# Optimization experiments

Measured on AMD Instinct MI355X. Metric: run time of the kernel, lower is better.

Reference implementation:

```python
import jax, jax.numpy as jnp
import numpy as np


def _conv(x, w, b=None, stride=1, pad=0):
    y = jax.lax.conv_general_dilated(x, w, (stride, stride), [(pad, pad), (pad, pad)],
                                     dimension_numbers=('NCHW', 'OIHW', 'NCHW'))
    if b is not None:
        y = y + b[None, :, None, None]
    return y


def _slice3d(grid, guide):
    # Trilinear grid_sample, align_corners=False, zero padding.
    # grid: (N, C=12, D=8, GH, GW); guide: (N,1,H,W) in [-1,1]
    N, C, D, GH, GW = grid.shape
    H, W = guide.shape[2], guide.shape[3]
    xs = 2.0 * jnp.arange(W, dtype=grid.dtype) / max(W - 1, 1) - 1.0
    ys = 2.0 * jnp.arange(H, dtype=grid.dtype) / max(H - 1, 1) - 1.0
    gx = ((xs + 1.0) * GW - 1.0) * 0.5               # (W,)
    gy = ((ys + 1.0) * GH - 1.0) * 0.5               # (H,)
    gz = ((guide[:, 0] + 1.0) * D - 1.0) * 0.5       # (N,H,W)
    x0f = jnp.floor(gx); y0f = jnp.floor(gy); z0f = jnp.floor(gz)
    fx = gx - x0f; fy = gy - y0f; fz = gz - z0f
    x0 = x0f.astype(jnp.int32); y0 = y0f.astype(jnp.int32); z0 = z0f.astype(jnp.int32)
    gf = grid.reshape(N, C, D * GH * GW)

    def corner(zi, yi, xi, wz, wy, wx):
        mask = ((zi >= 0) & (zi < D)) & ((yi >= 0) & (yi < GH))[None, :, None] & ((xi >= 0) & (xi < GW))[None, None, :]
        zc = jnp.clip(zi, 0, D - 1); yc = jnp.clip(yi, 0, GH - 1); xc = jnp.clip(xi, 0, GW - 1)
        flat = zc * (GH * GW) + yc[None, :, None] * GW + xc[None, None, :]   # (N,H,W)
        v = jnp.take_along_axis(gf, flat.reshape(N, 1, H * W), axis=2).reshape(N, C, H, W)
        w = (wz * wy[None, :, None] * wx[None, None, :]) * mask.astype(grid.dtype)  # (N,H,W)
        return v * w[:, None]

    out = jnp.zeros((N, C, H, W), grid.dtype)
    for dz in (0, 1):
        for dy in (0, 1):
            for dx in (0, 1):
                out = out + corner(z0 + dz, y0 + dy, x0 + dx,
                                   fz if dz else 1.0 - fz,
                                   fy if dy else 1.0 - fy,
                                   fx if dx else 1.0 - fx)
    return out


def setup_inputs() -> dict:
    key = jax.random.key(0)
    ks = jax.random.split(key, 40)
    def w(i, shape):
        return jax.random.normal(ks[i], shape, jnp.float32) * 0.05
    return {
        'low_res': jax.random.uniform(ks[0], (4, 3, 256, 256), jnp.float32),
        'full_res': jax.random.uniform(ks[1], (4, 1, 1024, 1024), jnp.float32),
        'w0': w(2, (8, 3, 3, 3)), 'b0': w(3, (8,)),
        'w1': w(4, (16, 8, 3, 3)), 'b1': w(5, (16,)),
        'w2': w(6, (32, 16, 3, 3)), 'b2': w(7, (32,)),
        'w3': w(8, (64, 32, 3, 3)), 'b3': w(9, (64,)),
        'wl0': w(10, (64, 64, 3, 3)), 'bl0': w(11, (64,)),
        'wl1': w(12, (64, 64, 3, 3)),
        'wg1': w(13, (128, 64, 3, 3)), 'bg1': w(14, (128,)),
        'wg2': w(15, (256, 128, 3, 3)), 'bg2': w(16, (256,)),
        'wf1': w(17, (256, 448, 1, 1)), 'bf1': w(18, (256,)),
        'wf2': w(19, (128, 256, 1, 1)), 'bf2': w(20, (128,)),
        'wf3': w(21, (64, 128, 1, 1)), 'bf3': w(22, (64,)),
        'wlin': w(23, (96, 64, 1, 1)), 'blin': w(24, (96,)),
        'wgd1': w(25, (16, 1, 3, 3)), 'bgd1': w(26, (16,)),
        'wgd2': w(27, (1, 16, 1, 1)), 'bgd2': w(28, (1,)),
        'wau1': w(29, (16, 1, 1, 1)), 'bau1': w(30, (16,)),
        'wau2': w(31, (1, 16, 1, 1)), 'bau2': w(32, (1,)),
        'wav1': w(33, (16, 1, 1, 1)), 'bav1': w(34, (16,)),
        'wav2': w(35, (1, 16, 1, 1)), 'bav2': w(36, (1,)),
    }


def reference(low_res, full_res, w0, b0, w1, b1, w2, b2, w3, b3, wl0, bl0, wl1,
              wg1, bg1, wg2, bg2, wf1, bf1, wf2, bf2, wf3, bf3, wlin, blin,
              wgd1, bgd1, wgd2, bgd2, wau1, bau1, wau2, bau2, wav1, bav1, wav2, bav2):
    relu = jax.nn.relu
    N = low_res.shape[0]
    H, W = full_res.shape[2], full_res.shape[3]
    fake = jax.image.resize(low_res, (N, 3, H, W), 'bilinear')
    # splat stack: 4 stride-2 convs
    x = relu(_conv(low_res, w0, b0, 2, 1))
    x = relu(_conv(x, w1, b1, 2, 1))
    x = relu(_conv(x, w2, b2, 2, 1))
    splat = relu(_conv(x, w3, b3, 2, 1))                 # (N,64,16,16)
    local = _conv(relu(_conv(splat, wl0, bl0, 1, 1)), wl1, None, 1, 1)
    # global branch
    a0 = splat.mean(axis=(2, 3), keepdims=True)
    x1 = relu(_conv(splat, wg1, bg1, 2, 1))
    a1 = x1.mean(axis=(2, 3), keepdims=True)
    x2 = relu(_conv(x1, wg2, bg2, 2, 1))
    a2 = x2.mean(axis=(2, 3), keepdims=True)
    a = jnp.concatenate([a0, a1, a2], axis=1)            # (N,448,1,1)
    a = relu(_conv(a, wf1, bf1))
    a = relu(_conv(a, wf2, bf2))
    glob = relu(_conv(a, wf3, bf3))                      # (N,64,1,1)
    fused = relu(glob + local)
    fused = _conv(fused, wlin, blin)                     # (N,96,16,16)
    grid = fused.reshape(N, 12, 8, fused.shape[2], fused.shape[3])
    guidemap = jnp.tanh(_conv(relu(_conv(full_res, wgd1, bgd1, 1, 1)), wgd2, bgd2))
    coeff = _slice3d(grid, guidemap)                     # (N,12,H,W)
    Y = full_res * coeff[:, 3:4] + coeff[:, 0:3].sum(axis=1, keepdims=True)
    U0 = full_res * coeff[:, 7:8] + coeff[:, 4:7].sum(axis=1, keepdims=True)
    V0 = full_res * coeff[:, 11:12] + coeff[:, 8:11].sum(axis=1, keepdims=True)
    U = jnp.tanh(_conv(relu(_conv(U0, wau1, bau1)), wau2, bau2)) + fake[:, 1:2]
    V = jnp.tanh(_conv(relu(_conv(V0, wav1, bav1)), wav2, bav2)) + fake[:, 2:3]
    return jnp.concatenate([Y, U, V], axis=1)
```

## Files before the change

### kernel.cpp

```cpp
#include <hip/hip_runtime.h>
#include <math.h>


__device__ __forceinline__ float tanh_fast(float x) {
    float e = __expf(2.0f * x);
    return 1.0f - 2.0f / (e + 1.0f);
}

__global__ __launch_bounds__(256) void conv3x3_s2_relu(
    const float* __restrict__ in, const float* __restrict__ w,
    const float* __restrict__ b, float* __restrict__ out,
    int N, int Cin, int Hin, int Win, int Cout, int Hout, int Wout)
{
    int idx = blockIdx.x * blockDim.x + threadIdx.x;
    int total = N * Cout * Hout * Wout;
    if (idx >= total) return;
    int wo = idx % Wout; int t = idx / Wout;
    int ho = t % Hout; t /= Hout;
    int co = t % Cout; int n = t / Cout;
    float acc = b[co];
    int hi0 = ho * 2 - 1, wi0 = wo * 2 - 1;
    const float* wp = w + (size_t)co * Cin * 9;
    for (int ci = 0; ci < Cin; ++ci) {
        const float* ip = in + ((size_t)(n * Cin + ci)) * Hin * Win;
        const float* wc = wp + ci * 9;
        #pragma unroll
        for (int kh = 0; kh < 3; ++kh) {
            int hi = hi0 + kh;
            if ((unsigned)hi >= (unsigned)Hin) continue;
            const float* row = ip + hi * Win;
            #pragma unroll
            for (int kw = 0; kw < 3; ++kw) {
                int wi = wi0 + kw;
                if ((unsigned)wi >= (unsigned)Win) continue;
                acc = fmaf(wc[kh * 3 + kw], row[wi], acc);
            }
        }
    }
    out[idx] = fmaxf(acc, 0.0f);
}

template<int CIN, int STRIDE, bool RELU, bool HASB>
__global__ __launch_bounds__(256) void conv_split(
    const float* __restrict__ in, const float* __restrict__ w,
    const float* __restrict__ b, float* __restrict__ out,
    int Cout, int Hin, int Win, int Hout, int Wout)
{
    constexpr int CPT = CIN / 4;
    int part = threadIdx.x >> 6;
    int lane = threadIdx.x & 63;
    int o = (blockIdx.x << 6) | lane;
    int wo = o % Wout; int t = o / Wout;
    int ho = t % Hout; t /= Hout;
    int co = t % Cout; int n = t / Cout;
    int hi0 = ho * STRIDE - 1, wi0 = wo * STRIDE - 1;
    const float* wp = w + ((size_t)co * CIN + part * CPT) * 9;
    const float* ip = in + ((size_t)n * CIN + part * CPT) * Hin * Win;
    float acc = 0.0f;
    for (int ci = 0; ci < CPT; ++ci) {
        const float* ic = ip + (size_t)ci * Hin * Win;
        const float* wc = wp + ci * 9;
        #pragma unroll
        for (int kh = 0; kh < 3; ++kh) {
            int hi = hi0 + kh;
            if ((unsigned)hi >= (unsigned)Hin) continue;
            const float* row = ic + hi * Win;
            #pragma unroll
            for (int kw = 0; kw < 3; ++kw) {
                int wi = wi0 + kw;
                if ((unsigned)wi >= (unsigned)Win) continue;
                acc = fmaf(wc[kh * 3 + kw], row[wi], acc);
            }
        }
    }
    __shared__ float red[256];
    red[threadIdx.x] = acc;
    __syncthreads();
    if (part == 0) {
        float s = acc + red[64 + lane] + red[128 + lane] + red[192 + lane];
        if (HASB) s += b[co];
        if (RELU) s = fmaxf(s, 0.0f);
        out[o] = s;
    }
}

__global__ __launch_bounds__(256) void means_kernel(
    const float* __restrict__ splat, const float* __restrict__ x1,
    const float* __restrict__ x2, float* __restrict__ avec)
{
    int wid = blockIdx.x * 4 + (threadIdx.x >> 6);
    int lane = threadIdx.x & 63;
    int n = wid / 448; int c = wid % 448;
    float s = 0.0f; float scale;
    if (c < 64) {
        const float* p = splat + ((size_t)(n * 64 + c)) * 256;
        s = p[lane] + p[lane + 64] + p[lane + 128] + p[lane + 192];
        scale = 1.0f / 256.0f;
    } else if (c < 192) {
        const float* p = x1 + ((size_t)(n * 128 + (c - 64))) * 64;
        s = p[lane];
        scale = 1.0f / 64.0f;
    } else {
        const float* p = x2 + ((size_t)(n * 256 + (c - 192))) * 16;
        s = (lane < 16) ? p[lane] : 0.0f;
        scale = 1.0f / 16.0f;
    }
    #pragma unroll
    for (int off = 32; off; off >>= 1) s += __shfl_down(s, off, 64);
    if (lane == 0) avec[wid] = s * scale;
}

template<int INDIM>
__global__ __launch_bounds__(256) void fc_relu(
    const float* __restrict__ in, const float* __restrict__ w,
    const float* __restrict__ b, float* __restrict__ out, int rows)
{
    int wid = blockIdx.x * 4 + (threadIdx.x >> 6);
    int lane = threadIdx.x & 63;
    int row = wid % rows; int n = wid / rows;
    const float* wp = w + (size_t)row * INDIM;
    const float* ip = in + (size_t)n * INDIM;
    float s = 0.0f;
    #pragma unroll
    for (int i = lane; i < INDIM; i += 64) s = fmaf(wp[i], ip[i], s);
    #pragma unroll
    for (int off = 32; off; off >>= 1) s += __shfl_down(s, off, 64);
    if (lane == 0) out[n * rows + row] = fmaxf(s + b[row], 0.0f);
}

__global__ __launch_bounds__(256) void fuse_grid(
    const float* __restrict__ glob, const float* __restrict__ local,
    const float* __restrict__ wlin, const float* __restrict__ blin,
    float* __restrict__ grid)
{
    int idx = blockIdx.x * blockDim.x + threadIdx.x;
    int p = idx & 255; int k = (idx >> 8) % 96; int n = idx / (96 * 256);
    float acc = blin[k];
    const float* wp = wlin + k * 64;
    const float* gl = glob + n * 64;
    const float* lo = local + (size_t)n * 64 * 256 + p;
    for (int c = 0; c < 64; ++c)
        acc = fmaf(wp[c], fmaxf(gl[c] + lo[c * 256], 0.0f), acc);
    int ch = k >> 3; int z = k & 7;
    grid[(((size_t)(n * 8 + z)) * 256 + p) * 12 + ch] = acc;
}

__global__ __launch_bounds__(256) void hdr_out_v2(
    const float* __restrict__ full, const float* __restrict__ low,
    const float* __restrict__ grid,
    const float* __restrict__ wgd1, const float* __restrict__ bgd1,
    const float* __restrict__ wgd2, const float* __restrict__ bgd2,
    const float* __restrict__ wau1, const float* __restrict__ bau1,
    const float* __restrict__ wau2, const float* __restrict__ bau2,
    const float* __restrict__ wav1, const float* __restrict__ bav1,
    const float* __restrict__ wav2, const float* __restrict__ bav2,
    float* __restrict__ out)
{
    int tid = blockIdx.x * 256 + threadIdx.x;
    int x0 = (tid & 255) << 2;
    int y = (tid >> 8) & 1023;
    int n = tid >> 18;
    const float* fp = full + ((size_t)n << 20);

    float v[3][6];
    #pragma unroll
    for (int r = 0; r < 3; ++r) {
        int yy = y + r - 1;
        bool okr = (unsigned)yy < 1024u;
        const float* row = fp + (size_t)yy * 1024;
        if (okr) {
            float4 m = *(const float4*)(row + x0);
            v[r][1] = m.x; v[r][2] = m.y; v[r][3] = m.z; v[r][4] = m.w;
            v[r][0] = (x0 > 0) ? row[x0 - 1] : 0.0f;
            v[r][5] = (x0 < 1020) ? row[x0 + 4] : 0.0f;
        } else {
            #pragma unroll
            for (int j = 0; j < 6; ++j) v[r][j] = 0.0f;
        }
    }

    float gacc[4];
    float bb = bgd2[0];
    #pragma unroll
    for (int px = 0; px < 4; ++px) gacc[px] = bb;
    #pragma unroll
    for (int k = 0; k < 16; ++k) {
        const float* wk = wgd1 + k * 9;
        float w0 = wk[0], w1 = wk[1], w2 = wk[2];
        float w3 = wk[3], w4 = wk[4], w5 = wk[5];
        float w6 = wk[6], w7 = wk[7], w8 = wk[8];
        float bk = bgd1[k], wo = wgd2[k];
        #pragma unroll
        for (int px = 0; px < 4; ++px) {
            float h = bk;
            h = fmaf(w0, v[0][px], h); h = fmaf(w1, v[0][px + 1], h); h = fmaf(w2, v[0][px + 2], h);
            h = fmaf(w3, v[1][px], h); h = fmaf(w4, v[1][px + 1], h); h = fmaf(w5, v[1][px + 2], h);
            h = fmaf(w6, v[2][px], h); h = fmaf(w7, v[2][px + 1], h); h = fmaf(w8, v[2][px + 2], h);
            gacc[px] = fmaf(wo, fmaxf(h, 0.0f), gacc[px]);
        }
    }

    const float* gbase = grid + (size_t)n * 24576;
    float Yo[4], Uo[4], Vo[4];

    #pragma unroll
    for (int px = 0; px < 4; ++px) {
        int x = x0 + px;
        float g = tanh_fast(gacc[px]);

        float gxc = (x * (32.0f / 1023.0f) - 1.0f) * 0.5f;
        float gyc = (y * (32.0f / 1023.0f) - 1.0f) * 0.5f;
        float gzc = 4.0f * g + 3.5f;
        float x0f = floorf(gxc), y0f = floorf(gyc), z0f = floorf(gzc);
        float fx = gxc - x0f, fy = gyc - y0f, fz = gzc - z0f;
        int ix = (int)x0f, iy = (int)y0f, iz = (int)z0f;

        float wx0 = (ix >= 0 && ix < 16) ? (1.0f - fx) : 0.0f;
        float wx1 = (ix + 1 >= 0 && ix + 1 < 16) ? fx : 0.0f;
        float wy0 = (iy >= 0 && iy < 16) ? (1.0f - fy) : 0.0f;
        float wy1 = (iy + 1 >= 0 && iy + 1 < 16) ? fy : 0.0f;
        float wz0 = (iz >= 0 && iz < 8) ? (1.0f - fz) : 0.0f;
        float wz1 = (iz + 1 >= 0 && iz + 1 < 8) ? fz : 0.0f;
        int xi0 = min(max(ix, 0), 15), xi1 = min(max(ix + 1, 0), 15);
        int yi0 = min(max(iy, 0), 15), yi1 = min(max(iy + 1, 0), 15);
        int zi0 = min(max(iz, 0), 7),  zi1 = min(max(iz + 1, 0), 7);

        float w00 = wy0 * wx0, w01 = wy0 * wx1, w10 = wy1 * wx0, w11 = wy1 * wx1;
        int o00 = yi0 * 16 + xi0, o01 = yi0 * 16 + xi1;
        int o10 = yi1 * 16 + xi0, o11 = yi1 * 16 + xi1;
        int z0b = zi0 * 256, z1b = zi1 * 256;

        float acc[12];
        #pragma unroll
        for (int i = 0; i < 12; ++i) acc[i] = 0.0f;

        #define CORNER(OFF, WK) { \
            const float4* q = (const float4*)(gbase + (size_t)(OFF) * 12); \
            float wk_ = (WK); \
            float4 A = q[0], B = q[1], C = q[2]; \
            acc[0] = fmaf(wk_, A.x, acc[0]); acc[1] = fmaf(wk_, A.y, acc[1]); \
            acc[2] = fmaf(wk_, A.z, acc[2]); acc[3] = fmaf(wk_, A.w, acc[3]); \
            acc[4] = fmaf(wk_, B.x, acc[4]); acc[5] = fmaf(wk_, B.y, acc[5]); \
            acc[6] = fmaf(wk_, B.z, acc[6]); acc[7] = fmaf(wk_, B.w, acc[7]); \
            acc[8] = fmaf(wk_, C.x, acc[8]); acc[9] = fmaf(wk_, C.y, acc[9]); \
            acc[10] = fmaf(wk_, C.z, acc[10]); acc[11] = fmaf(wk_, C.w, acc[11]); }

        CORNER(z0b + o00, wz0 * w00)
        CORNER(z0b + o01, wz0 * w01)
        CORNER(z0b + o10, wz0 * w10)
        CORNER(z0b + o11, wz0 * w11)
        CORNER(z1b + o00, wz1 * w00)
        CORNER(z1b + o01, wz1 * w01)
        CORNER(z1b + o10, wz1 * w10)
        CORNER(z1b + o11, wz1 * w11)
        #undef CORNER

        float p = v[1][px + 1];
        float Yv = fmaf(p, acc[3],  acc[0] + acc[1] + acc[2]);
        float U0 = fmaf(p, acc[7],  acc[4] + acc[5] + acc[6]);
        float V0 = fmaf(p, acc[11], acc[8] + acc[9] + acc[10]);

        float uacc = bau2[0];
        #pragma unroll
        for (int k = 0; k < 16; ++k)
            uacc = fmaf(wau2[k], fmaxf(fmaf(wau1[k], U0, bau1[k]), 0.0f), uacc);
        float vacc = bav2[0];
        #pragma unroll
        for (int k = 0; k < 16; ++k)
            vacc = fmaf(wav2[k], fmaxf(fmaf(wav1[k], V0, bav1[k]), 0.0f), vacc);

        float sx = (x + 0.5f) * 0.25f - 0.5f;
        float sy = (y + 0.5f) * 0.25f - 0.5f;
        float sxf = floorf(sx), syf = floorf(sy);
        float fxl = sx - sxf, fyl = sy - syf;
        int jx0 = max((int)sxf, 0), jx1 = min((int)sxf + 1, 255);
        int jy0 = max((int)syf, 0), jy1 = min((int)syf + 1, 255);
        const float* lr1 = low + ((size_t)(n * 3 + 1)) * 65536;
        const float* lr2 = low + ((size_t)(n * 3 + 2)) * 65536;
        float f1 = (1.0f - fyl) * ((1.0f - fxl) * lr1[jy0 * 256 + jx0] + fxl * lr1[jy0 * 256 + jx1])
                 + fyl * ((1.0f - fxl) * lr1[jy1 * 256 + jx0] + fxl * lr1[jy1 * 256 + jx1]);
        float f2 = (1.0f - fyl) * ((1.0f - fxl) * lr2[jy0 * 256 + jx0] + fxl * lr2[jy0 * 256 + jx1])
                 + fyl * ((1.0f - fxl) * lr2[jy1 * 256 + jx0] + fxl * lr2[jy1 * 256 + jx1]);

        Yo[px] = Yv;
        Uo[px] = tanh_fast(uacc) + f1;
        Vo[px] = tanh_fast(vacc) + f2;
    }

    size_t base = ((size_t)n * 3) * 1048576 + (size_t)y * 1024 + x0;
    *(float4*)(out + base)            = make_float4(Yo[0], Yo[1], Yo[2], Yo[3]);
    *(float4*)(out + base + 1048576)  = make_float4(Uo[0], Uo[1], Uo[2], Uo[3]);
    *(float4*)(out + base + 2097152)  = make_float4(Vo[0], Vo[1], Vo[2], Vo[3]);
}

extern "C" void kernel_launch(void* const* d_in, const int* in_sizes, int n_in,
                              void* d_out, int out_size, void* d_ws, size_t ws_size,
                              hipStream_t stream)
{
    const float* low  = (const float*)d_in[0];
    const float* full = (const float*)d_in[1];
    const float* w0 = (const float*)d_in[2];  const float* b0 = (const float*)d_in[3];
    const float* w1 = (const float*)d_in[4];  const float* b1 = (const float*)d_in[5];
    const float* w2 = (const float*)d_in[6];  const float* b2 = (const float*)d_in[7];
    const float* w3 = (const float*)d_in[8];  const float* b3 = (const float*)d_in[9];
    const float* wl0 = (const float*)d_in[10]; const float* bl0 = (const float*)d_in[11];
    const float* wl1 = (const float*)d_in[12];
    const float* wg1 = (const float*)d_in[13]; const float* bg1 = (const float*)d_in[14];
    const float* wg2 = (const float*)d_in[15]; const float* bg2 = (const float*)d_in[16];
    const float* wf1 = (const float*)d_in[17]; const float* bf1 = (const float*)d_in[18];
    const float* wf2 = (const float*)d_in[19]; const float* bf2 = (const float*)d_in[20];
    const float* wf3 = (const float*)d_in[21]; const float* bf3 = (const float*)d_in[22];
    const float* wlin = (const float*)d_in[23]; const float* blin = (const float*)d_in[24];
    const float* wgd1 = (const float*)d_in[25]; const float* bgd1 = (const float*)d_in[26];
    const float* wgd2 = (const float*)d_in[27]; const float* bgd2 = (const float*)d_in[28];
    const float* wau1 = (const float*)d_in[29]; const float* bau1 = (const float*)d_in[30];
    const float* wau2 = (const float*)d_in[31]; const float* bau2 = (const float*)d_in[32];
    const float* wav1 = (const float*)d_in[33]; const float* bav1 = (const float*)d_in[34];
    const float* wav2 = (const float*)d_in[35]; const float* bav2 = (const float*)d_in[36];
    float* out = (float*)d_out;

    float* ws = (float*)d_ws;
    float* t0    = ws;
    float* t1    = t0 + 524288;
    float* t2    = t1 + 262144;
    float* splat = t2 + 131072;
    float* l0o   = splat + 65536;
    float* local = l0o + 65536;
    float* x1    = local + 65536;
    float* x2    = x1 + 32768;
    float* avec  = x2 + 16384;
    float* h1    = avec + 1792;
    float* h2    = h1 + 1024;
    float* glob  = h2 + 512;
    float* gridb = glob + 256;

    conv3x3_s2_relu<<<2048, 256, 0, stream>>>(low, w0, b0, t0, 4, 3, 256, 256, 8, 128, 128);
    conv3x3_s2_relu<<<1024, 256, 0, stream>>>(t0, w1, b1, t1, 4, 8, 128, 128, 16, 64, 64);
    conv_split<16, 2, true, true><<<2048, 256, 0, stream>>>(t1, w2, b2, t2, 32, 64, 64, 32, 32);
    conv_split<32, 2, true, true><<<1024, 256, 0, stream>>>(t2, w3, b3, splat, 64, 32, 32, 16, 16);
    conv_split<64, 1, true, true><<<1024, 256, 0, stream>>>(splat, wl0, bl0, l0o, 64, 16, 16, 16, 16);
    conv_split<64, 1, false, false><<<1024, 256, 0, stream>>>(l0o, wl1, nullptr, local, 64, 16, 16, 16, 16);
    conv_split<64, 2, true, true><<<512, 256, 0, stream>>>(splat, wg1, bg1, x1, 128, 16, 16, 8, 8);
    conv_split<128, 2, true, true><<<256, 256, 0, stream>>>(x1, wg2, bg2, x2, 256, 8, 8, 4, 4);
    means_kernel<<<448, 256, 0, stream>>>(splat, x1, x2, avec);
    fc_relu<448><<<256, 256, 0, stream>>>(avec, wf1, bf1, h1, 256);
    fc_relu<256><<<128, 256, 0, stream>>>(h1, wf2, bf2, h2, 128);
    fc_relu<128><<<64, 256, 0, stream>>>(h2, wf3, bf3, glob, 64);
    fuse_grid<<<384, 256, 0, stream>>>(glob, local, wlin, blin, gridb);
    hdr_out_v2<<<4096, 256, 0, stream>>>(full, low, gridb,
        wgd1, bgd1, wgd2, bgd2, wau1, bau1, wau2, bau2, wav1, bav1, wav2, bav2, out);
}
```

Baseline: 393.8 us.

## Fuse whole HDRNet pipeline into one persistent kernel with grid barriers

Replaces fourteen separate kernel launches with a single persistent kernel of 1024 blocks that walks through every stage and separates them with atomic-counter grid barriers. Independent conv branches are merged into the same phase, the three FC layers are collapsed into one per-batch block using shared memory, and the low-res bilinear upsample in the output stage is simplified to reuse three column samples across four pixels. This removes launch gaps and tail effects between small kernels, but relies on all 1024 blocks being co-resident for the spin barriers to work and forces a fixed grid size on the large output stage.

```diff
diff --git a/kernel.cpp b/kernel.cpp
--- a/kernel.cpp
+++ b/kernel.cpp
@@ -1,25 +1,38 @@
 #include <hip/hip_runtime.h>
 #include <math.h>
 
+
+#define NB 1024
+#define GSZ (NB * 256)
 
 __device__ __forceinline__ float tanh_fast(float x) {
     float e = __expf(2.0f * x);
     return 1.0f - 2.0f / (e + 1.0f);
 }
 
-__global__ __launch_bounds__(256) void conv3x3_s2_relu(
+__device__ __forceinline__ void gsync(int* bar, int id) {
+    __syncthreads();
+    if (threadIdx.x == 0) {
+        __threadfence();
+        int* c = bar + id * 32;
+        atomicAdd(c, 1);
+        int guard = 0;
+        while (__hip_atomic_load(c, __ATOMIC_RELAXED, __HIP_MEMORY_SCOPE_AGENT) < NB
+               && guard < (1 << 27)) {
+            ++guard;
+            __builtin_amdgcn_s_sleep(1);
+        }
+        __threadfence();
+    }
+    __syncthreads();
+}
+
+__device__ __forceinline__ float conv_tpo(
     const float* __restrict__ in, const float* __restrict__ w,
-    const float* __restrict__ b, float* __restrict__ out,
-    int N, int Cin, int Hin, int Win, int Cout, int Hout, int Wout)
+    int n, int co, int ho, int wo, int Cin, int Hin, int Win, int stride)
 {
-    int idx = blockIdx.x * blockDim.x + threadIdx.x;
-    int total = N * Cout * Hout * Wout;
-    if (idx >= total) return;
-    int wo = idx % Wout; int t = idx / Wout;
-    int ho = t % Hout; t /= Hout;
-    int co = t % Cout; int n = t / Cout;
-    float acc = b[co];
-    int hi0 = ho * 2 - 1, wi0 = wo * 2 - 1;
+    float acc = 0.0f;
+    int hi0 = ho * stride - 1, wi0 = wo * stride - 1;
     const float* wp = w + (size_t)co * Cin * 9;
     for (int ci = 0; ci < Cin; ++ci) {
         const float* ip = in + ((size_t)(n * Cin + ci)) * Hin * Win;
@@ -37,19 +50,19 @@
             }
         }
     }
-    out[idx] = fmaxf(acc, 0.0f);
+    return acc;
 }
 
 template<int CIN, int STRIDE, bool RELU, bool HASB>
-__global__ __launch_bounds__(256) void conv_split(
+__device__ __forceinline__ void conv_split_tb(
     const float* __restrict__ in, const float* __restrict__ w,
     const float* __restrict__ b, float* __restrict__ out,
-    int Cout, int Hin, int Win, int Hout, int Wout)
+    int tb, int Cout, int Hin, int Win, int Hout, int Wout, float* red)
 {
     constexpr int CPT = CIN / 4;
     int part = threadIdx.x >> 6;
     int lane = threadIdx.x & 63;
-    int o = (blockIdx.x << 6) | lane;
+    int o = (tb << 6) | lane;
     int wo = o % Wout; int t = o / Wout;
     int ho = t % Hout; t /= Hout;
     int co = t % Cout; int n = t / Cout;
@@ -73,7 +86,6 @@
             }
         }
     }
-    __shared__ float red[256];
     red[threadIdx.x] = acc;
     __syncthreads();
     if (part == 0) {
@@ -82,215 +94,316 @@
         if (RELU) s = fmaxf(s, 0.0f);
         out[o] = s;
     }
-}
-
-__global__ __launch_bounds__(256) void means_kernel(
-    const float* __restrict__ splat, const float* __restrict__ x1,
-    const float* __restrict__ x2, float* __restrict__ avec)
-{
-    int wid = blockIdx.x * 4 + (threadIdx.x >> 6);
-    int lane = threadIdx.x & 63;
-    int n = wid / 448; int c = wid % 448;
-    float s = 0.0f; float scale;
-    if (c < 64) {
-        const float* p = splat + ((size_t)(n * 64 + c)) * 256;
-        s = p[lane] + p[lane + 64] + p[lane + 128] + p[lane + 192];
-        scale = 1.0f / 256.0f;
-    } else if (c < 192) {
-        const float* p = x1 + ((size_t)(n * 128 + (c - 64))) * 64;
-        s = p[lane];
-        scale = 1.0f / 64.0f;
-    } else {
-        const float* p = x2 + ((size_t)(n * 256 + (c - 192))) * 16;
-        s = (lane < 16) ? p[lane] : 0.0f;
-        scale = 1.0f / 16.0f;
-    }
-    #pragma unroll
-    for (int off = 32; off; off >>= 1) s += __shfl_down(s, off, 64);
-    if (lane == 0) avec[wid] = s * scale;
-}
-
-template<int INDIM>
-__global__ __launch_bounds__(256) void fc_relu(
-    const float* __restrict__ in, const float* __restrict__ w,
-    const float* __restrict__ b, float* __restrict__ out, int rows)
-{
-    int wid = blockIdx.x * 4 + (threadIdx.x >> 6);
-    int lane = threadIdx.x & 63;
-    int row = wid % rows; int n = wid / rows;
-    const float* wp = w + (size_t)row * INDIM;
-    const float* ip = in + (size_t)n * INDIM;
-    float s = 0.0f;
-    #pragma unroll
-    for (int i = lane; i < INDIM; i += 64) s = fmaf(wp[i], ip[i], s);
-    #pragma unroll
-    for (int off = 32; off; off >>= 1) s += __shfl_down(s, off, 64);
-    if (lane == 0) out[n * rows + row] = fmaxf(s + b[row], 0.0f);
-}
-
-__global__ __launch_bounds__(256) void fuse_grid(
-    const float* __restrict__ glob, const float* __restrict__ local,
+    __syncthreads();
+}
+
+__global__ __launch_bounds__(256, 4) void hdrnet_mega(
+    const float* __restrict__ low, const float* __restrict__ full,
+    const float* __restrict__ w0, const float* __restrict__ b0,
+    const float* __restrict__ w1, const float* __restrict__ b1,
+    const float* __restrict__ w2, const float* __restrict__ b2,
+    const float* __restrict__ w3, const float* __restrict__ b3,
+    const float* __restrict__ wl0, const float* __restrict__ bl0,
+    const float* __restrict__ wl1,
+    const float* __restrict__ wg1, const float* __restrict__ bg1,
+    const float* __restrict__ wg2, const float* __restrict__ bg2,
+    const float* __restrict__ wf1, const float* __restrict__ bf1,
+    const float* __restrict__ wf2, const float* __restrict__ bf2,
+    const float* __restrict__ wf3, const float* __restrict__ bf3,
     const float* __restrict__ wlin, const float* __restrict__ blin,
-    float* __restrict__ grid)
-{
-    int idx = blockIdx.x * blockDim.x + threadIdx.x;
-    int p = idx & 255; int k = (idx >> 8) % 96; int n = idx / (96 * 256);
-    float acc = blin[k];
-    const float* wp = wlin + k * 64;
-    const float* gl = glob + n * 64;
-    const float* lo = local + (size_t)n * 64 * 256 + p;
-    for (int c = 0; c < 64; ++c)
-        acc = fmaf(wp[c], fmaxf(gl[c] + lo[c * 256], 0.0f), acc);
-    int ch = k >> 3; int z = k & 7;
-    grid[(((size_t)(n * 8 + z)) * 256 + p) * 12 + ch] = acc;
-}
-
-__global__ __launch_bounds__(256) void hdr_out_v2(
-    const float* __restrict__ full, const float* __restrict__ low,
-    const float* __restrict__ grid,
     const float* __restrict__ wgd1, const float* __restrict__ bgd1,
     const float* __restrict__ wgd2, const float* __restrict__ bgd2,
     const float* __restrict__ wau1, const float* __restrict__ bau1,
     const float* __restrict__ wau2, const float* __restrict__ bau2,
     const float* __restrict__ wav1, const float* __restrict__ bav1,
     const float* __restrict__ wav2, const float* __restrict__ bav2,
-    float* __restrict__ out)
+    float* __restrict__ out, int* __restrict__ bar, float* __restrict__ wsf)
 {
-    int tid = blockIdx.x * 256 + threadIdx.x;
-    int x0 = (tid & 255) << 2;
-    int y = (tid >> 8) & 1023;
-    int n = tid >> 18;
-    const float* fp = full + ((size_t)n << 20);
-
-    float v[3][6];
-    #pragma unroll
-    for (int r = 0; r < 3; ++r) {
-        int yy = y + r - 1;
-        bool okr = (unsigned)yy < 1024u;
-        const float* row = fp + (size_t)yy * 1024;
-        if (okr) {
-            float4 m = *(const float4*)(row + x0);
-            v[r][1] = m.x; v[r][2] = m.y; v[r][3] = m.z; v[r][4] = m.w;
-            v[r][0] = (x0 > 0) ? row[x0 - 1] : 0.0f;
-            v[r][5] = (x0 < 1020) ? row[x0 + 4] : 0.0f;
-        } else {
-            #pragma unroll
-            for (int j = 0; j < 6; ++j) v[r][j] = 0.0f;
-        }
-    }
-
-    float gacc[4];
-    float bb = bgd2[0];
-    #pragma unroll
-    for (int px = 0; px < 4; ++px) gacc[px] = bb;
-    #pragma unroll
-    for (int k = 0; k < 16; ++k) {
-        const float* wk = wgd1 + k * 9;
-        float w0 = wk[0], w1 = wk[1], w2 = wk[2];
-        float w3 = wk[3], w4 = wk[4], w5 = wk[5];
-        float w6 = wk[6], w7 = wk[7], w8 = wk[8];
-        float bk = bgd1[k], wo = wgd2[k];
-        #pragma unroll
-        for (int px = 0; px < 4; ++px) {
-            float h = bk;
-            h = fmaf(w0, v[0][px], h); h = fmaf(w1, v[0][px + 1], h); h = fmaf(w2, v[0][px + 2], h);
-            h = fmaf(w3, v[1][px], h); h = fmaf(w4, v[1][px + 1], h); h = fmaf(w5, v[1][px + 2], h);
-            h = fmaf(w6, v[2][px], h); h = fmaf(w7, v[2][px + 1], h); h = fmaf(w8, v[2][px + 2], h);
-            gacc[px] = fmaf(wo, fmaxf(h, 0.0f), gacc[px]);
-        }
-    }
-
-    const float* gbase = grid + (size_t)n * 24576;
-    float Yo[4], Uo[4], Vo[4];
-
-    #pragma unroll
-    for (int px = 0; px < 4; ++px) {
-        int x = x0 + px;
-        float g = tanh_fast(gacc[px]);
-
-        float gxc = (x * (32.0f / 1023.0f) - 1.0f) * 0.5f;
+    __shared__ float smem[848];
+    float* red = smem;
+    const int tid = blockIdx.x * 256 + threadIdx.x;
+
+    float* t0b    = wsf;
+    float* t1b    = t0b + 524288;
+    float* t2b    = t1b + 262144;
+    float* splat  = t2b + 131072;
+    float* l0o    = splat + 65536;
+    float* localb = l0o + 65536;
+    float* x1b    = localb + 65536;
+    float* x2b    = x1b + 32768;
+    float* avec   = x2b + 16384;
+    float* glob   = avec + 1792;
+    float* gridb  = glob + 256;
+
+    for (int idx = tid; idx < 524288; idx += GSZ) {
+        int wo = idx & 127; int t = idx >> 7;
+        int ho = t & 127; t >>= 7;
+        int co = t & 7; int n = t >> 3;
+        float acc = conv_tpo(low, w0, n, co, ho, wo, 3, 256, 256, 2) + b0[co];
+        t0b[idx] = fmaxf(acc, 0.0f);
+    }
+    gsync(bar, 0);
+
+    if (tid < 262144) {
+        int wo = tid & 63; int t = tid >> 6;
+        int ho = t & 63; t >>= 6;
+        int co = t & 15; int n = t >> 4;
+        float acc = conv_tpo(t0b, w1, n, co, ho, wo, 8, 128, 128, 2) + b1[co];
+        t1b[tid] = fmaxf(acc, 0.0f);
+    }
+    gsync(bar, 1);
+
+    if (tid < 131072) {
+        int wo = tid & 31; int t = tid >> 5;
+        int ho = t & 31; t >>= 5;
+        int co = t & 31; int n = t >> 5;
+        float acc = conv_tpo(t1b, w2, n, co, ho, wo, 16, 64, 64, 2) + b2[co];
+        t2b[tid] = fmaxf(acc, 0.0f);
+    }
+    gsync(bar, 2);
+
+    conv_split_tb<32, 2, true, true>(t2b, w3, b3, splat, blockIdx.x, 64, 32, 32, 16, 16, red);
+    gsync(bar, 3);
+
+    for (int tb = blockIdx.x; tb < 1536; tb += NB) {
+        if (tb < 1024)
+            conv_split_tb<64, 1, true, true>(splat, wl0, bl0, l0o, tb, 64, 16, 16, 16, 16, red);
+        else
+            conv_split_tb<64, 2, true, true>(splat, wg1, bg1, x1b, tb - 1024, 128, 16, 16, 8, 8, red);
+    }
+    gsync(bar, 4);
+
+    for (int tb = blockIdx.x; tb < 1280; tb += NB) {
+        if (tb < 1024)
+            conv_split_tb<64, 1, false, false>(l0o, wl1, nullptr, localb, tb, 64, 16, 16, 16, 16, red);
+        else
+            conv_split_tb<128, 2, true, true>(x1b, wg2, bg2, x2b, tb - 1024, 256, 8, 8, 4, 4, red);
+    }
+    gsync(bar, 5);
+
+    {
+        int wid = blockIdx.x * 4 + (threadIdx.x >> 6);
+        int lane = threadIdx.x & 63;
+        if (wid < 1792) {
+            int n = wid / 448; int c = wid % 448;
+            float s = 0.0f; float scale;
+            if (c < 64) {
+                const float* p = splat + ((size_t)(n * 64 + c)) * 256;
+                s = p[lane] + p[lane + 64] + p[lane + 128] + p[lane + 192];
+                scale = 1.0f / 256.0f;
+            } else if (c < 192) {
+                const float* p = x1b + ((size_t)(n * 128 + (c - 64))) * 64;
+                s = p[lane];
+                scale = 1.0f / 64.0f;
+            } else {
+                const float* p = x2b + ((size_t)(n * 256 + (c - 192))) * 16;
+                s = (lane < 16) ? p[lane] : 0.0f;
+                scale = 1.0f / 16.0f;
+            }
+            #pragma unroll
+            for (int off = 32; off; off >>= 1) s += __shfl_down(s, off, 64);
+            if (lane == 0) avec[wid] = s * scale;
+        }
+    }
+    gsync(bar, 6);
+
+    if (blockIdx.x < 4) {
+        int n = blockIdx.x, t = threadIdx.x;
+        float* a   = smem;
+        float* hh1 = smem + 448;
+        float* hh2 = smem + 704;
+        if (t < 224) { a[t] = avec[n * 448 + t]; a[t + 224] = avec[n * 448 + t + 224]; }
+        __syncthreads();
+        {
+            float a0 = 0, a1 = 0, a2 = 0, a3 = 0;
+            const float* wp = wf1 + (size_t)t * 448;
+            for (int i = 0; i < 448; i += 4) {
+                a0 = fmaf(wp[i], a[i], a0); a1 = fmaf(wp[i + 1], a[i + 1], a1);
+                a2 = fmaf(wp[i + 2], a[i + 2], a2); a3 = fmaf(wp[i + 3], a[i + 3], a3);
+            }
+            float s = a0 + a1 + a2 + a3 + bf1[t];
+            __syncthreads();
+            hh1[t] = fmaxf(s, 0.0f);
+        }
+        __syncthreads();
+        if (t < 128) {
+            float a0 = 0, a1 = 0, a2 = 0, a3 = 0;
+            const float* wp = wf2 + (size_t)t * 256;
+            for (int i = 0; i < 256; i += 4) {
+                a0 = fmaf(wp[i], hh1[i], a0); a1 = fmaf(wp[i + 1], hh1[i + 1], a1);
+                a2 = fmaf(wp[i + 2], hh1[i + 2], a2); a3 = fmaf(wp[i + 3], hh1[i + 3], a3);
+            }
+            hh2[t] = fmaxf(a0 + a1 + a2 + a3 + bf2[t], 0.0f);
+        }
+        __syncthreads();
+        if (t < 64) {
+            float a0 = 0, a1 = 0, a2 = 0, a3 = 0;
+            const float* wp = wf3 + (size_t)t * 128;
+            for (int i = 0; i < 128; i += 4) {
+                a0 = fmaf(wp[i], hh2[i], a0); a1 = fmaf(wp[i + 1], hh2[i + 1], a1);
+                a2 = fmaf(wp[i + 2], hh2[i + 2], a2); a3 = fmaf(wp[i + 3], hh2[i + 3], a3);
+            }
+            glob[n * 64 + t] = fmaxf(a0 + a1 + a2 + a3 + bf3[t], 0.0f);
+        }
+    }
+    gsync(bar, 7);
+
+    if (tid < 98304) {
+        int p = tid & 255; int k = (tid >> 8) % 96; int n = tid / (96 * 256);
+        float acc = blin[k];
+        const float* wp = wlin + k * 64;
+        const float* gl = glob + n * 64;
+        const float* lo = localb + (size_t)n * 64 * 256 + p;
+        for (int c = 0; c < 64; ++c)
+            acc = fmaf(wp[c], fmaxf(gl[c] + lo[c * 256], 0.0f), acc);
+        int ch = k >> 3; int z = k & 7;
+        gridb[(((size_t)(n * 8 + z)) * 256 + p) * 12 + ch] = acc;
+    }
+    gsync(bar, 8);
+
+    for (int t = tid; t < 1048576; t += GSZ) {
+        int x0 = (t & 255) << 2;
+        int y = (t >> 8) & 1023;
+        int n = t >> 18;
+        const float* fp = full + ((size_t)n << 20);
+
+        float v[3][6];
+        #pragma unroll
+        for (int r = 0; r < 3; ++r) {
+            int yy = y + r - 1;
+            bool okr = (unsigned)yy < 1024u;
+            const float* row = fp + (size_t)yy * 1024;
+            if (okr) {
+                float4 m = *(const float4*)(row + x0);
+                v[r][1] = m.x; v[r][2] = m.y; v[r][3] = m.z; v[r][4] = m.w;
+                v[r][0] = (x0 > 0) ? row[x0 - 1] : 0.0f;
+                v[r][5] = (x0 < 1020) ? row[x0 + 4] : 0.0f;
+            } else {
+                #pragma unroll
+                for (int j = 0; j < 6; ++j) v[r][j] = 0.0f;
+            }
+        }
+
+        float gacc[4];
+        float bb = bgd2[0];
+        #pragma unroll
+        for (int px = 0; px < 4; ++px) gacc[px] = bb;
+        #pragma unroll
+        for (int k = 0; k < 16; ++k) {
+            const float* wk = wgd1 + k * 9;
+            float q0 = wk[0], q1 = wk[1], q2 = wk[2];
+            float q3 = wk[3], q4 = wk[4], q5 = wk[5];
+            float q6 = wk[6], q7 = wk[7], q8 = wk[8];
+            float bk = bgd1[k], wo = wgd2[k];
+            #pragma unroll
+            for (int px = 0; px < 4; ++px) {
+                float h = bk;
+                h = fmaf(q0, v[0][px], h); h = fmaf(q1, v[0][px + 1], h); h = fmaf(q2, v[0][px + 2], h);
+                h = fmaf(q3, v[1][px], h); h = fmaf(q4, v[1][px + 1], h); h = fmaf(q5, v[1][px + 2], h);
+                h = fmaf(q6, v[2][px], h); h = fmaf(q7, v[2][px + 1], h); h = fmaf(q8, v[2][px + 2], h);
+                gacc[px] = fmaf(wo, fmaxf(h, 0.0f), gacc[px]);
+            }
+        }
+
         float gyc = (y * (32.0f / 1023.0f) - 1.0f) * 0.5f;
-        float gzc = 4.0f * g + 3.5f;
-        float x0f = floorf(gxc), y0f = floorf(gyc), z0f = floorf(gzc);
-        float fx = gxc - x0f, fy = gyc - y0f, fz = gzc - z0f;
-        int ix = (int)x0f, iy = (int)y0f, iz = (int)z0f;
-
-        float wx0 = (ix >= 0 && ix < 16) ? (1.0f - fx) : 0.0f;
-        float wx1 = (ix + 1 >= 0 && ix + 1 < 16) ? fx : 0.0f;
+        float y0f = floorf(gyc); float fy = gyc - y0f; int iy = (int)y0f;
         float wy0 = (iy >= 0 && iy < 16) ? (1.0f - fy) : 0.0f;
-        float wy1 = (iy + 1 >= 0 && iy + 1 < 16) ? fy : 0.0f;
-        float wz0 = (iz >= 0 && iz < 8) ? (1.0f - fz) : 0.0f;
-        float wz1 = (iz + 1 >= 0 && iz + 1 < 8) ? fz : 0.0f;
-        int xi0 = min(max(ix, 0), 15), xi1 = min(max(ix + 1, 0), 15);
-        int yi0 = min(max(iy, 0), 15), yi1 = min(max(iy + 1, 0), 15);
-        int zi0 = min(max(iz, 0), 7),  zi1 = min(max(iz + 1, 0), 7);
-
-        float w00 = wy0 * wx0, w01 = wy0 * wx1, w10 = wy1 * wx0, w11 = wy1 * wx1;
-        int o00 = yi0 * 16 + xi0, o01 = yi0 * 16 + xi1;
-        int o10 = yi1 * 16 + xi0, o11 = yi1 * 16 + xi1;
-        int z0b = zi0 * 256, z1b = zi1 * 256;
-
-        float acc[12];
-        #pragma unroll
-        for (int i = 0; i < 12; ++i) acc[i] = 0.0f;
-
-        #define CORNER(OFF, WK) { \
-            const float4* q = (const float4*)(gbase + (size_t)(OFF) * 12); \
-            float wk_ = (WK); \
-            float4 A = q[0], B = q[1], C = q[2]; \
-            acc[0] = fmaf(wk_, A.x, acc[0]); acc[1] = fmaf(wk_, A.y, acc[1]); \
-            acc[2] = fmaf(wk_, A.z, acc[2]); acc[3] = fmaf(wk_, A.w, acc[3]); \
-            acc[4] = fmaf(wk_, B.x, acc[4]); acc[5] = fmaf(wk_, B.y, acc[5]); \
-            acc[6] = fmaf(wk_, B.z, acc[6]); acc[7] = fmaf(wk_, B.w, acc[7]); \
-            acc[8] = fmaf(wk_, C.x, acc[8]); acc[9] = fmaf(wk_, C.y, acc[9]); \
-            acc[10] = fmaf(wk_, C.z, acc[10]); acc[11] = fmaf(wk_, C.w, acc[11]); }
-
-        CORNER(z0b + o00, wz0 * w00)
-        CORNER(z0b + o01, wz0 * w01)
-        CORNER(z0b + o10, wz0 * w10)
-        CORNER(z0b + o11, wz0 * w11)
-        CORNER(z1b + o00, wz1 * w00)
-        CORNER(z1b + o01, wz1 * w01)
-        CORNER(z1b + o10, wz1 * w10)
-        CORNER(z1b + o11, wz1 * w11)
-        #undef CORNER
-
-        float p = v[1][px + 1];
-        float Yv = fmaf(p, acc[3],  acc[0] + acc[1] + acc[2]);
-        float U0 = fmaf(p, acc[7],  acc[4] + acc[5] + acc[6]);
-        float V0 = fmaf(p, acc[11], acc[8] + acc[9] + acc[10]);
-
-        float uacc = bau2[0];
-        #pragma unroll
-        for (int k = 0; k < 16; ++k)
-            uacc = fmaf(wau2[k], fmaxf(fmaf(wau1[k], U0, bau1[k]), 0.0f), uacc);
-        float vacc = bav2[0];
-        #pragma unroll
-        for (int k = 0; k < 16; ++k)
-            vacc = fmaf(wav2[k], fmaxf(fmaf(wav1[k], V0, bav1[k]), 0.0f), vacc);
-
-        float sx = (x + 0.5f) * 0.25f - 0.5f;
+        float wy1 = (iy + 1 < 16) ? fy : 0.0f;
+        int yi0 = min(max(iy, 0), 15), yi1 = min(iy + 1, 15);
+
         float sy = (y + 0.5f) * 0.25f - 0.5f;
-        float sxf = floorf(sx), syf = floorf(sy);
-        float fxl = sx - sxf, fyl = sy - syf;
-        int jx0 = max((int)sxf, 0), jx1 = min((int)sxf + 1, 255);
+        float syf = floorf(sy); float fyl = sy - syf;
         int jy0 = max((int)syf, 0), jy1 = min((int)syf + 1, 255);
+        int jc = x0 >> 2;
+        int c0 = max(jc - 1, 0), c2 = min(jc + 1, 255);
         const float* lr1 = low + ((size_t)(n * 3 + 1)) * 65536;
         const float* lr2 = low + ((size_t)(n * 3 + 2)) * 65536;
-        float f1 = (1.0f - fyl) * ((1.0f - fxl) * lr1[jy0 * 256 + jx0] + fxl * lr1[jy0 * 256 + jx1])
-                 + fyl * ((1.0f - fxl) * lr1[jy1 * 256 + jx0] + fxl * lr1[jy1 * 256 + jx1]);
-        float f2 = (1.0f - fyl) * ((1.0f - fxl) * lr2[jy0 * 256 + jx0] + fxl * lr2[jy0 * 256 + jx1])
-                 + fyl * ((1.0f - fxl) * lr2[jy1 * 256 + jx0] + fxl * lr2[jy1 * 256 + jx1]);
-
-        Yo[px] = Yv;
-        Uo[px] = tanh_fast(uacc) + f1;
-        Vo[px] = tanh_fast(vacc) + f2;
-    }
-
-    size_t base = ((size_t)n * 3) * 1048576 + (size_t)y * 1024 + x0;
-    *(float4*)(out + base)            = make_float4(Yo[0], Yo[1], Yo[2], Yo[3]);
-    *(float4*)(out + base + 1048576)  = make_float4(Uo[0], Uo[1], Uo[2], Uo[3]);
-    *(float4*)(out + base + 2097152)  = make_float4(Vo[0], Vo[1], Vo[2], Vo[3]);
+        float ua = lr1[jy0 * 256 + c0] + fyl * (lr1[jy1 * 256 + c0] - lr1[jy0 * 256 + c0]);
+        float ub = lr1[jy0 * 256 + jc] + fyl * (lr1[jy1 * 256 + jc] - lr1[jy0 * 256 + jc]);
+        float uc = lr1[jy0 * 256 + c2] + fyl * (lr1[jy1 * 256 + c2] - lr1[jy0 * 256 + c2]);
+        float va = lr2[jy0 * 256 + c0] + fyl * (lr2[jy1 * 256 + c0] - lr2[jy0 * 256 + c0]);
+        float vb = lr2[jy0 * 256 + jc] + fyl * (lr2[jy1 * 256 + jc] - lr2[jy0 * 256 + jc]);
+        float vc = lr2[jy0 * 256 + c2] + fyl * (lr2[jy1 * 256 + c2] - lr2[jy0 * 256 + c2]);
+        const float cfx[4] = {0.625f, 0.875f, 0.125f, 0.375f};
+
+        const float* gbase = gridb + (size_t)n * 24576;
+        float Yo[4], Uo[4], Vo[4];
+
+        #pragma unroll
+        for (int px = 0; px < 4; ++px) {
+            int x = x0 + px;
+            float g = tanh_fast(gacc[px]);
+
+            float gxc = (x * (32.0f / 1023.0f) - 1.0f) * 0.5f;
+            float gzc = 4.0f * g + 3.5f;
+            float x0f = floorf(gxc), z0f = floorf(gzc);
+            float fx = gxc - x0f, fz = gzc - z0f;
+            int ix = (int)x0f, iz = (int)z0f;
+
+            float wx0 = (ix >= 0 && ix < 16) ? (1.0f - fx) : 0.0f;
+            float wx1 = (ix + 1 < 16) ? fx : 0.0f;
+            float wz0 = (iz >= 0 && iz < 8) ? (1.0f - fz) : 0.0f;
+            float wz1 = (iz + 1 >= 0 && iz + 1 < 8) ? fz : 0.0f;
+            int xi0 = min(max(ix, 0), 15), xi1 = min(ix + 1, 15);
+            int zi0 = min(max(iz, 0), 7),  zi1 = min(max(iz + 1, 0), 7);
+
+            float w00 = wy0 * wx0, w01 = wy0 * wx1, w10 = wy1 * wx0, w11 = wy1 * wx1;
+            int o00 = yi0 * 16 + xi0, o01 = yi0 * 16 + xi1;
+            int o10 = yi1 * 16 + xi0, o11 = yi1 * 16 + xi1;
+            int z0b = zi0 * 256, z1b = zi1 * 256;
+
+            float acc[12];
+            #pragma unroll
+            for (int i = 0; i < 12; ++i) acc[i] = 0.0f;
+
+            #define CORNER(OFF, WK) { \
+                const float4* q = (const float4*)(gbase + (size_t)(OFF) * 12); \
+                float wk_ = (WK); \
+                float4 A = q[0], B = q[1], C = q[2]; \
+                acc[0] = fmaf(wk_, A.x, acc[0]); acc[1] = fmaf(wk_, A.y, acc[1]); \
+                acc[2] = fmaf(wk_, A.z, acc[2]); acc[3] = fmaf(wk_, A.w, acc[3]); \
+                acc[4] = fmaf(wk_, B.x, acc[4]); acc[5] = fmaf(wk_, B.y, acc[5]); \
+                acc[6] = fmaf(wk_, B.z, acc[6]); acc[7] = fmaf(wk_, B.w, acc[7]); \
+                acc[8] = fmaf(wk_, C.x, acc[8]); acc[9] = fmaf(wk_, C.y, acc[9]); \
+                acc[10] = fmaf(wk_, C.z, acc[10]); acc[11] = fmaf(wk_, C.w, acc[11]); }
+
+            CORNER(z0b + o00, wz0 * w00)
+            CORNER(z0b + o01, wz0 * w01)
+            CORNER(z0b + o10, wz0 * w10)
+            CORNER(z0b + o11, wz0 * w11)
+            CORNER(z1b + o00, wz1 * w00)
+            CORNER(z1b + o01, wz1 * w01)
+            CORNER(z1b + o10, wz1 * w10)
+            CORNER(z1b + o11, wz1 * w11)
+            #undef CORNER
+
+            float p = v[1][px + 1];
+            float Yv = fmaf(p, acc[3],  acc[0] + acc[1] + acc[2]);
+            float U0 = fmaf(p, acc[7],  acc[4] + acc[5] + acc[6]);
+            float V0 = fmaf(p, acc[11], acc[8] + acc[9] + acc[10]);
+
+            float uacc = bau2[0];
+            #pragma unroll
+            for (int k = 0; k < 16; ++k)
+                uacc = fmaf(wau2[k], fmaxf(fmaf(wau1[k], U0, bau1[k]), 0.0f), uacc);
+            float vacc = bav2[0];
+            #pragma unroll
+            for (int k = 0; k < 16; ++k)
+                vacc = fmaf(wav2[k], fmaxf(fmaf(wav1[k], V0, bav1[k]), 0.0f), vacc);
+
+            float f1 = (px < 2) ? (ua + cfx[px] * (ub - ua)) : (ub + cfx[px] * (uc - ub));
+            float f2 = (px < 2) ? (va + cfx[px] * (vb - va)) : (vb + cfx[px] * (vc - vb));
+
+            Yo[px] = Yv;
+            Uo[px] = tanh_fast(uacc) + f1;
+            Vo[px] = tanh_fast(vacc) + f2;
+        }
+
+        size_t base = ((size_t)n * 3) * 1048576 + (size_t)y * 1024 + x0;
+        *(float4*)(out + base)            = make_float4(Yo[0], Yo[1], Yo[2], Yo[3]);
+        *(float4*)(out + base + 1048576)  = make_float4(Uo[0], Uo[1], Uo[2], Uo[3]);
+        *(float4*)(out + base + 2097152)  = make_float4(Vo[0], Vo[1], Vo[2], Vo[3]);
+    }
 }
 
 extern "C" void kernel_launch(void* const* d_in, const int* in_sizes, int n_in,
@@ -319,34 +432,13 @@
     const float* wav2 = (const float*)d_in[35]; const float* bav2 = (const float*)d_in[36];
     float* out = (float*)d_out;
 
-    float* ws = (float*)d_ws;
-    float* t0    = ws;
-    float* t1    = t0 + 524288;
-    float* t2    = t1 + 262144;
-    float* splat = t2 + 131072;
-    float* l0o   = splat + 65536;
-    float* local = l0o + 65536;
-    float* x1    = local + 65536;
-    float* x2    = x1 + 32768;
-    float* avec  = x2 + 16384;
-    float* h1    = avec + 1792;
-    float* h2    = h1 + 1024;
-    float* glob  = h2 + 512;
-    float* gridb = glob + 256;
-
-    conv3x3_s2_relu<<<2048, 256, 0, stream>>>(low, w0, b0, t0, 4, 3, 256, 256, 8, 128, 128);
-    conv3x3_s2_relu<<<1024, 256, 0, stream>>>(t0, w1, b1, t1, 4, 8, 128, 128, 16, 64, 64);
-    conv_split<16, 2, true, true><<<2048, 256, 0, stream>>>(t1, w2, b2, t2, 32, 64, 64, 32, 32);
-    conv_split<32, 2, true, true><<<1024, 256, 0, stream>>>(t2, w3, b3, splat, 64, 32, 32, 16, 16);
-    conv_split<64, 1, true, true><<<1024, 256, 0, stream>>>(splat, wl0, bl0, l0o, 64, 16, 16, 16, 16);
-    conv_split<64, 1, false, false><<<1024, 256, 0, stream>>>(l0o, wl1, nullptr, local, 64, 16, 16, 16, 16);
-    conv_split<64, 2, true, true><<<512, 256, 0, stream>>>(splat, wg1, bg1, x1, 128, 16, 16, 8, 8);
-    conv_split<128, 2, true, true><<<256, 256, 0, stream>>>(x1, wg2, bg2, x2, 256, 8, 8, 4, 4);
-    means_kernel<<<448, 256, 0, stream>>>(splat, x1, x2, avec);
-    fc_relu<448><<<256, 256, 0, stream>>>(avec, wf1, bf1, h1, 256);
-    fc_relu<256><<<128, 256, 0, stream>>>(h1, wf2, bf2, h2, 128);
-    fc_relu<128><<<64, 256, 0, stream>>>(h2, wf3, bf3, glob, 64);
-    fuse_grid<<<384, 256, 0, stream>>>(glob, local, wlin, blin, gridb);
-    hdr_out_v2<<<4096, 256, 0, stream>>>(full, low, gridb,
-        wgd1, bgd1, wgd2, bgd2, wau1, bau1, wau2, bau2, wav1, bav1, wav2, bav2, out);
-}
+    int* bar = (int*)d_ws;
+    float* wsf = (float*)d_ws + 1024;
+
+    hipMemsetAsync(bar, 0, 4096, stream);
+    hdrnet_mega<<<NB, 256, 0, stream>>>(
+        low, full, w0, b0, w1, b1, w2, b2, w3, b3, wl0, bl0, wl1,
+        wg1, bg1, wg2, bg2, wf1, bf1, wf2, bf2, wf3, bf3, wlin, blin,
+        wgd1, bgd1, wgd2, bgd2, wau1, bau1, wau2, bau2, wav1, bav1, wav2, bav2,
+        out, bar, wsf);
+}
```

Measured after the change: 1.287 ms. +226.9%, slower.
